# Optimization experiments

Hardware: AMD Instinct MI355X
Metric: run time of the kernel (lower is better)

## Reference

```python
import jax, jax.numpy as jnp
import numpy as np

NUM_NODES = 100000
NUM_EDGES = 600000
NUM_GRAPHS = 512
D = 128  # num_features == latent widths


def setup_inputs() -> dict:
    key = jax.random.key(0)
    ks = jax.random.split(key, 16)
    inp = {
        "x": jax.random.normal(ks[0], (NUM_NODES, D), dtype=jnp.float32),
        "edge_index": jax.random.randint(ks[1], (2, NUM_EDGES), 0, NUM_NODES, dtype=jnp.int32),
        "batch": jnp.sort(jax.random.randint(ks[2], (NUM_NODES,), 0, NUM_GRAPHS, dtype=jnp.int32)),
    }
    s = 1.0 / np.sqrt(D)
    # SAGEConv params per layer: lin_l (applied to mean-aggregated neighbors), lin_r (root), bias
    for i in range(3):
        inp[f"Wl{i+1}"] = jax.random.uniform(ks[3 + 3 * i], (D, D), jnp.float32, -s, s)
        inp[f"Wr{i+1}"] = jax.random.uniform(ks[4 + 3 * i], (D, D), jnp.float32, -s, s)
        inp[f"b{i+1}"] = jax.random.uniform(ks[5 + 3 * i], (D,), jnp.float32, -s, s)
    inp["Wro"] = jax.random.uniform(ks[12], (D, 1), jnp.float32, -s, s)
    inp["bro"] = jax.random.uniform(ks[13], (1,), jnp.float32, -s, s)
    return inp


def _sage_conv(h, Wl, Wr, b, src, dst):
    # mean aggregation of source features at destination nodes
    msg = jax.ops.segment_sum(h[src], dst, num_segments=NUM_NODES)          # [N, D]
    cnt = jax.ops.segment_sum(jnp.ones((src.shape[0], 1), h.dtype), dst,
                              num_segments=NUM_NODES)                        # [N, 1]
    mean = msg / jnp.maximum(cnt, 1.0)
    return mean @ Wl + h @ Wr + b


def reference(x, edge_index, batch, Wl1, Wr1, b1, Wl2, Wr2, b2, Wl3, Wr3, b3, Wro, bro):
    src, dst = edge_index[0], edge_index[1]
    h = x
    for Wl, Wr, b in ((Wl1, Wr1, b1), (Wl2, Wr2, b2), (Wl3, Wr3, b3)):
        h = jax.nn.relu(_sage_conv(h, Wl, Wr, b, src, dst))
    # per-graph sum pooling (replaces the python loop over unique batch ids)
    pooled = jax.ops.segment_sum(h, batch, num_segments=NUM_GRAPHS)  # [G, D]
    return jax.nn.sigmoid(pooled @ Wro + bro)  # [G, 1]
```

## Files before the change

### kernel.cpp

```cpp
#include <hip/hip_runtime.h>
#include <math.h>

#define N_NODES 100000
#define N_EDGES 600000
#define N_GRAPHS 512
#define D 128
#define SCAN_BS 1024
#define SCAN_NBC ((N_NODES + SCAN_BS - 1) / SCAN_BS)
#define NPART 8
#define PART_SZ (N_NODES / NPART)
#define E4 (N_EDGES / 4)
#define SPLIT_B 12500

typedef unsigned short u16;
typedef __attribute__((ext_vector_type(8))) short short8;
typedef __attribute__((ext_vector_type(4))) float f32x4;

__device__ __forceinline__ u16 f2bf(float f) {
    unsigned int u = __float_as_uint(f);
    u += 0x7FFFu + ((u >> 16) & 1u);
    return (u16)(u >> 16);
}
__device__ __forceinline__ float bf2f(u16 h) {
    return __uint_as_float(((unsigned int)h) << 16);
}
__device__ __forceinline__ void split2(float f, unsigned int& h16, unsigned int& l16) {
    unsigned int u = __float_as_uint(f);
    unsigned int hb = (u + (0x7FFFu + ((u >> 16) & 1u))) & 0xffff0000u;
    float lo = f - __uint_as_float(hb);
    unsigned int ul = __float_as_uint(lo);
    h16 = hb >> 16;
    l16 = (ul + (0x7FFFu + ((ul >> 16) & 1u))) >> 16;
}

typedef __attribute__((address_space(1))) const unsigned int gas_u32;
typedef __attribute__((address_space(3))) unsigned int las_u32;
__device__ __forceinline__ void gload16(const void* g, void* l) {
    __builtin_amdgcn_global_load_lds((gas_u32*)g, (las_u32*)l, 16, 0, 0);
}

__global__ __launch_bounds__(256) void zero_i_kernel(int* __restrict__ p, int n) {
    int i = blockIdx.x * 256 + threadIdx.x;
    if (i < n) p[i] = 0;
}

__global__ __launch_bounds__(256) void hist_kernel(const int* __restrict__ dst,
                                                   int* __restrict__ deg) {
    int e = blockIdx.x * 256 + threadIdx.x;
    if (e < N_EDGES) atomicAdd(&deg[dst[e]], 1);
}

__global__ __launch_bounds__(1024) void scan1_kernel(const int* __restrict__ deg,
                                                     int* __restrict__ excl,
                                                     int* __restrict__ blocksum) {
    __shared__ int buf[2][SCAN_BS];
    const int t = threadIdx.x;
    const int gid = blockIdx.x * SCAN_BS + t;
    int v = (gid < N_NODES) ? deg[gid] : 0;
    buf[0][t] = v;
    __syncthreads();
    int pi = 0;
    for (int off = 1; off < SCAN_BS; off <<= 1) {
        int val = buf[pi][t];
        if (t >= off) val += buf[pi][t - off];
        buf[pi ^ 1][t] = val;
        pi ^= 1;
        __syncthreads();
    }
    int incl = buf[pi][t];
    if (gid < N_NODES) excl[gid] = incl - v;
    if (t == SCAN_BS - 1) blocksum[blockIdx.x] = incl;
}

__global__ __launch_bounds__(256) void scan3_kernel(const int* __restrict__ excl,
                                                    const int* __restrict__ blocksum,
                                                    int* __restrict__ rowptr) {
    __shared__ int buf[2][128];
    const int t = threadIdx.x;
    if (t < 128) buf[0][t] = (t < SCAN_NBC) ? blocksum[t] : 0;
    __syncthreads();
    int pi = 0;
    for (int off = 1; off < 128; off <<= 1) {
        if (t < 128) {
            int val = buf[pi][t];
            if (t >= off) val += buf[pi][t - off];
            buf[pi ^ 1][t] = val;
        }
        pi ^= 1;
        __syncthreads();
    }
    const int i = blockIdx.x * 256 + t;
    if (i < N_NODES) {
        const int j = i / SCAN_BS;
        const int pref = (j == 0) ? 0 : buf[pi][j - 1];
        rowptr[i] = excl[i] + pref;
    }
    if (i == 0) rowptr[N_NODES] = N_EDGES;
}

__global__ __launch_bounds__(256) void fill_kernel(const int* __restrict__ src,
                                                   const int* __restrict__ dst,
                                                   const int* __restrict__ rowptr,
                                                   int* __restrict__ fill,
                                                   int* __restrict__ csr_src) {
    const int lo = (blockIdx.x & (NPART - 1)) * PART_SZ;
    const int i4 = (blockIdx.x >> 3) * 256 + threadIdx.x;
    if (i4 >= E4) return;
    const int4 d4 = ((const int4*)dst)[i4];
    const int4 s4 = ((const int4*)src)[i4];
    if ((unsigned)(d4.x - lo) < (unsigned)PART_SZ) {
        int pos = rowptr[d4.x] + atomicAdd(&fill[d4.x], 1);
        csr_src[pos] = s4.x;
    }
    if ((unsigned)(d4.y - lo) < (unsigned)PART_SZ) {
        int pos = rowptr[d4.y] + atomicAdd(&fill[d4.y], 1);
        csr_src[pos] = s4.y;
    }
    if ((unsigned)(d4.z - lo) < (unsigned)PART_SZ) {
        int pos = rowptr[d4.z] + atomicAdd(&fill[d4.z], 1);
        csr_src[pos] = s4.z;
    }
    if ((unsigned)(d4.w - lo) < (unsigned)PART_SZ) {
        int pos = rowptr[d4.w] + atomicAdd(&fill[d4.w], 1);
        csr_src[pos] = s4.w;
    }
}

__global__ __launch_bounds__(256) void prep_kernel(const float* __restrict__ x,
                                                   u16* __restrict__ Hhi,
                                                   u16* __restrict__ Hlo,
                                                   const float* __restrict__ Wl1, const float* __restrict__ Wr1,
                                                   const float* __restrict__ Wl2, const float* __restrict__ Wr2,
                                                   const float* __restrict__ Wl3, const float* __restrict__ Wr3,
                                                   u16* __restrict__ wph, u16* __restrict__ wpl) {
    if (blockIdx.x < SPLIT_B) {
        const int i = blockIdx.x * 256 + threadIdx.x;
        const float4 v = ((const float4*)x)[i];
        unsigned int h0, l0, h1, l1, h2, l2, h3, l3;
        split2(v.x, h0, l0); split2(v.y, h1, l1);
        split2(v.z, h2, l2); split2(v.w, h3, l3);
        uint2 oh, ol;
        oh.x = h0 | (h1 << 16); oh.y = h2 | (h3 << 16);
        ol.x = l0 | (l1 << 16); ol.y = l2 | (l3 << 16);
        ((uint2*)Hhi)[i] = oh;
        ((uint2*)Hlo)[i] = ol;
    } else {
        const int b = (blockIdx.x - SPLIT_B) * 4 + (threadIdx.x >> 6);
        const int lane = threadIdx.x & 63;
        const int layer = b >> 6;
        const int t = b & 63;
        const float* Wl = (layer == 0) ? Wl1 : (layer == 1) ? Wl2 : Wl3;
        const float* Wr = (layer == 0) ? Wr1 : (layer == 1) ? Wr2 : Wr3;
        const int nt = t >> 3, kt = t & 7;
        const int n = nt * 16 + (lane & 15);
        const int k0 = kt * 32 + (lane >> 4) * 8;
        const size_t base = (size_t)layer * 32768 + (size_t)(t * 64 + lane) * 8;
        #pragma unroll
        for (int j = 0; j < 8; ++j) {
            const int k = k0 + j;
            const float w = (k < 128) ? Wl[k * 128 + n] : Wr[(k - 128) * 128 + n];
            const u16 h = f2bf(w);
            wph[base + j] = h;
            wpl[base + j] = f2bf(w - bf2f(h));
        }
    }
}

__global__ __launch_bounds__(512, 4) void gemm_kernel(const u16* __restrict__ INhi,
                                                      const u16* __restrict__ INlo,
                                                      const int* __restrict__ rowptr,
                                                      const int* __restrict__ csr_src,
                                                      const u16* __restrict__ Wph,
                                                      const u16* __restrict__ Wpl,
                                                      const float* __restrict__ bias,
                                                      u16* __restrict__ OHhi,
                                                      u16* __restrict__ OHlo,
                                                      const float* __restrict__ Wro,
                                                      float* rowdot) {
    __shared__ uint4 ldsAll[5120];
    const int t = threadIdx.x;
    const int lane = t & 63;
    const int wv = t >> 6;
    const int m0 = blockIdx.x * 128 + wv * 16;
    const int row16 = m0 + (lane & 15);
    int rm = row16; if (rm >= N_NODES) rm = 0;
    const int ko = (lane >> 4) * 8;

    int beg = 0, deg = 0;
    if (row16 < N_NODES) {
        beg = rowptr[row16];
        deg = rowptr[row16 + 1] - beg;
    }

#define STAGE_W(Q, B) do {                                                      \
        const uint4* gh_ = (const uint4*)Wph + (Q) * 1024;                      \
        const uint4* gl_ = (const uint4*)Wpl + (Q) * 1024;                      \
        _Pragma("unroll")                                                       \
        for (int i_ = 0; i_ < 2; ++i_) {                                        \
            gload16(gh_ + t + 512 * i_,                                         \
                    (void*)&ldsAll[(B) * 2048 + wv * 64 + 512 * i_]);           \
            gload16(gl_ + t + 512 * i_,                                         \
                    (void*)&ldsAll[(B) * 2048 + 1024 + wv * 64 + 512 * i_]);    \
        }                                                                       \
    } while (0)

    STAGE_W(0, 0);
    __builtin_amdgcn_sched_barrier(0);
    STAGE_W(1, 1);
    __builtin_amdgcn_sched_barrier(0);

    short8 ah[4], al[4];
    #pragma unroll
    for (int kt = 0; kt < 4; ++kt) {
        ah[kt] = *(const short8*)(INhi + (size_t)rm * D + kt * 32 + ko);
        al[kt] = *(const short8*)(INlo + (size_t)rm * D + kt * 32 + ko);
    }

    float ac[4][8];
    #pragma unroll
    for (int kt = 0; kt < 4; ++kt) {
        #pragma unroll
        for (int j = 0; j < 8; ++j) ac[kt][j] = 0.f;
    }
    int s_cur = (deg > 0) ? csr_src[beg] : 0;
    for (int n = 0; __any(n < deg); ++n) {
        const bool act = n < deg;
        const int s_nxt = (n + 1 < deg) ? csr_src[beg + n + 1] : 0;
        if (act) {
            const size_t rb = (size_t)s_cur * D + ko;
            #pragma unroll
            for (int kt = 0; kt < 4; ++kt) {
                const uint4 v = *(const uint4*)(INhi + rb + kt * 32);
                ac[kt][0] += __uint_as_float(v.x << 16);
                ac[kt][1] += __uint_as_float(v.x & 0xffff0000u);
                ac[kt][2] += __uint_as_float(v.y << 16);
                ac[kt][3] += __uint_as_float(v.y & 0xffff0000u);
                ac[kt][4] += __uint_as_float(v.z << 16);
                ac[kt][5] += __uint_as_float(v.z & 0xffff0000u);
                ac[kt][6] += __uint_as_float(v.w << 16);
                ac[kt][7] += __uint_as_float(v.w & 0xffff0000u);
            }
        }
        s_cur = s_nxt;
    }
    const float inv = 1.0f / (float)max(deg, 1);
    short8 am[4];
    #pragma unroll
    for (int kt = 0; kt < 4; ++kt) {
        uint4 u;
        u.x = (unsigned)f2bf(ac[kt][0] * inv) | ((unsigned)f2bf(ac[kt][1] * inv) << 16);
        u.y = (unsigned)f2bf(ac[kt][2] * inv) | ((unsigned)f2bf(ac[kt][3] * inv) << 16);
        u.z = (unsigned)f2bf(ac[kt][4] * inv) | ((unsigned)f2bf(ac[kt][5] * inv) << 16);
        u.w = (unsigned)f2bf(ac[kt][6] * inv) | ((unsigned)f2bf(ac[kt][7] * inv) << 16);
        am[kt] = __builtin_bit_cast(short8, u);
    }
    __builtin_amdgcn_sched_barrier(0);

    const int cl = lane & 15;
    const int g4 = (lane >> 4) << 2;
    char* bounceB = (char*)ldsAll + 65536 + wv * 2048;

    f32x4 acc8[2][4];

#define COMPUTE_S(Q, B) do {                                                    \
        const u16* bufU_ = (const u16*)(ldsAll + (B) * 2048);                   \
        _Pragma("unroll")                                                       \
        for (int l_ = 0; l_ < 2; ++l_) {                                        \
            f32x4 acc_ = {0.f, 0.f, 0.f, 0.f};                                  \
            _Pragma("unroll")                                                   \
            for (int kt_ = 0; kt_ < 8; ++kt_) {                                 \
                const int fo_ = (l_ * 8 + kt_) * 512 + lane * 8;                \
                const short8 bh_ = *(const short8*)(bufU_ + fo_);               \
                const short8 bl_ = *(const short8*)(bufU_ + 8192 + fo_);        \
                if (kt_ < 4) {                                                  \
                    acc_ = __builtin_amdgcn_mfma_f32_16x16x32_bf16(am[kt_], bh_, acc_, 0, 0, 0); \
                    acc_ = __builtin_amdgcn_mfma_f32_16x16x32_bf16(am[kt_], bl_, acc_, 0, 0, 0); \
                } else {                                                        \
                    acc_ = __builtin_amdgcn_mfma_f32_16x16x32_bf16(ah[kt_ - 4], bh_, acc_, 0, 0, 0); \
                    acc_ = __builtin_amdgcn_mfma_f32_16x16x32_bf16(ah[kt_ - 4], bl_, acc_, 0, 0, 0); \
                    acc_ = __builtin_amdgcn_mfma_f32_16x16x32_bf16(al[kt_ - 4], bh_, acc_, 0, 0, 0); \
                }                                                               \
            }                                                                   \
            acc8[(Q) >> 1][((Q) & 1) * 2 + l_] = acc_;                          \
        }                                                                       \
    } while (0)

    asm volatile("s_waitcnt vmcnt(0)" ::: "memory");
    __builtin_amdgcn_s_barrier();
    COMPUTE_S(0, 0);
    __builtin_amdgcn_s_barrier();
    STAGE_W(2, 0);
    COMPUTE_S(1, 1);
    __builtin_amdgcn_s_barrier();
    STAGE_W(3, 1);
    asm volatile("s_waitcnt vmcnt(4)" ::: "memory");
    __builtin_amdgcn_s_barrier();
    COMPUTE_S(2, 0);
    asm volatile("s_waitcnt vmcnt(0)" ::: "memory");
    __builtin_amdgcn_s_barrier();
    COMPUTE_S(3, 1);

    if (rowdot) {
        float wsum[4] = {0.f, 0.f, 0.f, 0.f};
        #pragma unroll
        for (int si = 0; si < 2; ++si) {
            #pragma unroll
            for (int nt2 = 0; nt2 < 4; ++nt2) {
                const int col = (si * 4 + nt2) * 16 + cl;
                const float bv = bias[col];
                const float wroc = Wro[col];
                #pragma unroll
                for (int r = 0; r < 4; ++r) {
                    const float v = fmaxf(acc8[si][nt2][r] + bv, 0.f);
                    wsum[r] = fmaf(v, wroc, wsum[r]);
                }
            }
        }
        #pragma unroll
        for (int r = 0; r < 4; ++r) {
            float tsum = wsum[r];
            tsum += __shfl_down(tsum, 8, 64);
            tsum += __shfl_down(tsum, 4, 64);
            tsum += __shfl_down(tsum, 2, 64);
            tsum += __shfl_down(tsum, 1, 64);
            const int row = m0 + g4 + r;
            if (cl == 0 && row < N_NODES) {
                rowdot[row] = tsum;
            }
        }
    } else {
        #pragma unroll
        for (int si = 0; si < 2; ++si) {
            asm volatile("s_waitcnt lgkmcnt(0)" ::: "memory");
            unsigned int lo_pack[8];
            #pragma unroll
            for (int nt2 = 0; nt2 < 4; ++nt2) {
                const int col = (si * 4 + nt2) * 16 + cl;
                const float bv = bias[col];
                #pragma unroll
                for (int r = 0; r < 4; ++r) {
                    const int rr = g4 + r;
                    const float v = fmaxf(acc8[si][nt2][r] + bv, 0.f);
                    unsigned int h16, l16;
                    split2(v, h16, l16);
                    const int boff = (rr * 128 + (nt2 * 16 + cl) * 2) ^ ((rr & 7) << 4);
                    *(u16*)(bounceB + boff) = (u16)h16;
                    if (r & 1) lo_pack[nt2 * 2 + (r >> 1)] |= l16 << 16;
                    else       lo_pack[nt2 * 2 + (r >> 1)]  = l16;
                }
            }
            asm volatile("s_waitcnt lgkmcnt(0)" ::: "memory");
            #pragma unroll
            for (int j = 0; j < 2; ++j) {
                const int rr = j * 8 + (lane >> 3);
                const int blk = lane & 7;
                const uint4 vv = *(const uint4*)(bounceB + rr * 128 + ((blk ^ (rr & 7)) << 4));
                const int grow = m0 + rr;
                if (grow < N_NODES)
                    *(uint4*)(OHhi + (size_t)grow * D + si * 64 + blk * 8) = vv;
            }
            asm volatile("s_waitcnt lgkmcnt(0)" ::: "memory");
            #pragma unroll
            for (int nt2 = 0; nt2 < 4; ++nt2) {
                #pragma unroll
                for (int r = 0; r < 4; ++r) {
                    const int rr = g4 + r;
                    const unsigned int l16 = (lo_pack[nt2 * 2 + (r >> 1)] >> ((r & 1) * 16)) & 0xffffu;
                    const int boff = (rr * 128 + (nt2 * 16 + cl) * 2) ^ ((rr & 7) << 4);
                    *(u16*)(bounceB + boff) = (u16)l16;
                }
            }
            asm volatile("s_waitcnt lgkmcnt(0)" ::: "memory");
            #pragma unroll
            for (int j = 0; j < 2; ++j) {
                const int rr = j * 8 + (lane >> 3);
                const int blk = lane & 7;
                const uint4 vv = *(const uint4*)(bounceB + rr * 128 + ((blk ^ (rr & 7)) << 4));
                const int grow = m0 + rr;
                if (grow < N_NODES)
                    *(uint4*)(OHlo + (size_t)grow * D + si * 64 + blk * 8) = vv;
            }
        }
    }
#undef STAGE_W
#undef COMPUTE_S
}

__global__ __launch_bounds__(64) void final_kernel(const float* __restrict__ rowdot,
                                                   const int* __restrict__ batch,
                                                   const float* __restrict__ bro,
                                                   float* __restrict__ out) {
    const int g = blockIdx.x;
    const int t = threadIdx.x;
    int lo = 0, hi = N_NODES;
    while (lo < hi) { int mid = (lo + hi) >> 1; if (batch[mid] < g) lo = mid + 1; else hi = mid; }
    int lo2 = lo, hi2 = N_NODES;
    while (lo2 < hi2) { int mid = (lo2 + hi2) >> 1; if (batch[mid] < g + 1) lo2 = mid + 1; else hi2 = mid; }

    float acc = 0.0f;
    for (int i = lo + t; i < lo2; i += 64) acc += rowdot[i];
    #pragma unroll
    for (int off = 32; off > 0; off >>= 1) acc += __shfl_down(acc, off, 64);
    if (t == 0) out[g] = 1.0f / (1.0f + expf(-(acc + bro[0])));
}

extern "C" void kernel_launch(void* const* d_in, const int* in_sizes, int n_in,
                              void* d_out, int out_size, void* d_ws, size_t ws_size,
                              hipStream_t stream) {
    const float* x     = (const float*)d_in[0];
    const int*   ei    = (const int*)d_in[1];
    const int*   batch = (const int*)d_in[2];
    const int*   src   = ei;
    const int*   dst   = ei + N_EDGES;
    const float* Wl[3] = {(const float*)d_in[3], (const float*)d_in[6], (const float*)d_in[9]};
    const float* Wr[3] = {(const float*)d_in[4], (const float*)d_in[7], (const float*)d_in[10]};
    const float* bs[3] = {(const float*)d_in[5], (const float*)d_in[8], (const float*)d_in[11]};
    const float* Wro   = (const float*)d_in[12];
    const float* bro   = (const float*)d_in[13];
    float* out = (float*)d_out;

    const size_t ND = (size_t)N_NODES * D;
    char* ws = (char*)d_ws;
    u16* Ahi = (u16*)ws;
    u16* Alo = Ahi + ND;
    u16* Bhi = Alo + ND;
    u16* Blo = Bhi + ND;
    u16* Wph = Blo + ND;
    u16* Wpl = Wph + 3 * 32768;
    int* deg      = (int*)(Wpl + 3 * 32768);
    int* fill     = deg + N_NODES;
    float* rowdot = (float*)(fill + N_NODES);
    int* excl     = (int*)(rowdot + N_NODES);
    int* blocksum = excl + N_NODES;
    int* rowptr   = blocksum + 128;
    int* csr_src  = rowptr + N_NODES + 1;

    const int EB      = (N_EDGES + 255) / 256;
    const int NB      = (N_NODES + 255) / 256;
    const int NB2     = (2 * N_NODES + 255) / 256;
    const int EPB     = ((E4 + 255) / 256) * NPART;
    const int PREP_B  = SPLIT_B + 48;
    const int GEMM_B  = (N_NODES + 127) / 128;

    zero_i_kernel<<<NB2, 256, 0, stream>>>(deg, 2 * N_NODES);
    hist_kernel<<<EB, 256, 0, stream>>>(dst, deg);
    scan1_kernel<<<SCAN_NBC, SCAN_BS, 0, stream>>>(deg, excl, blocksum);
    scan3_kernel<<<NB, 256, 0, stream>>>(excl, blocksum, rowptr);
    fill_kernel<<<EPB, 256, 0, stream>>>(src, dst, rowptr, fill, csr_src);

    prep_kernel<<<PREP_B, 256, 0, stream>>>(x, Ahi, Alo,
                                            Wl[0], Wr[0], Wl[1], Wr[1], Wl[2], Wr[2],
                                            Wph, Wpl);

    gemm_kernel<<<GEMM_B, 512, 0, stream>>>(Ahi, Alo, rowptr, csr_src,
                                            Wph, Wpl, bs[0],
                                            Bhi, Blo, Wro, (float*)nullptr);
    gemm_kernel<<<GEMM_B, 512, 0, stream>>>(Bhi, Blo, rowptr, csr_src,
                                            Wph + 32768, Wpl + 32768, bs[1],
                                            Ahi, Alo, Wro, (float*)nullptr);
    gemm_kernel<<<GEMM_B, 512, 0, stream>>>(Ahi, Alo, rowptr, csr_src,
                                            Wph + 2 * 32768, Wpl + 2 * 32768, bs[2],
                                            Bhi, Blo, Wro, rowdot);

    final_kernel<<<N_GRAPHS, 64, 0, stream>>>(rowdot, batch, bro, out);
}
```

Baseline: 363.6 us.

## Halve weight staging chunks to shrink LDS footprint and deepen pipeline

Weight staging into LDS now uses 8 chunks of 16 output columns each instead of 4 chunks of 32, so the shared buffer shrinks from 80 KB to 32 KB. The bounce buffer is moved to alias the weight buffers after compute finishes. The aim is to raise occupancy per CU, since the launch bounds ask for 4 blocks of 512 threads. In exchange there are more barriers and waitcnt stages, with less compute between each load and its use.

```diff
diff --git a/kernel.cpp b/kernel.cpp
--- a/kernel.cpp
+++ b/kernel.cpp
@@ -177,7 +177,7 @@
                                                       u16* __restrict__ OHlo,
                                                       const float* __restrict__ Wro,
                                                       float* rowdot) {
-    __shared__ uint4 ldsAll[5120];
+    __shared__ uint4 ldsAll[2048];
     const int t = threadIdx.x;
     const int lane = t & 63;
     const int wv = t >> 6;
@@ -193,15 +193,10 @@
     }
 
 #define STAGE_W(Q, B) do {                                                      \
-        const uint4* gh_ = (const uint4*)Wph + (Q) * 1024;                      \
-        const uint4* gl_ = (const uint4*)Wpl + (Q) * 1024;                      \
-        _Pragma("unroll")                                                       \
-        for (int i_ = 0; i_ < 2; ++i_) {                                        \
-            gload16(gh_ + t + 512 * i_,                                         \
-                    (void*)&ldsAll[(B) * 2048 + wv * 64 + 512 * i_]);           \
-            gload16(gl_ + t + 512 * i_,                                         \
-                    (void*)&ldsAll[(B) * 2048 + 1024 + wv * 64 + 512 * i_]);    \
-        }                                                                       \
+        const uint4* gh_ = (const uint4*)Wph + (Q) * 512;                       \
+        const uint4* gl_ = (const uint4*)Wpl + (Q) * 512;                       \
+        gload16(gh_ + t, (void*)&ldsAll[(B) * 1024 + wv * 64]);                 \
+        gload16(gl_ + t, (void*)&ldsAll[(B) * 1024 + 512 + wv * 64]);           \
     } while (0)
 
     STAGE_W(0, 0);
@@ -258,31 +253,27 @@
 
     const int cl = lane & 15;
     const int g4 = (lane >> 4) << 2;
-    char* bounceB = (char*)ldsAll + 65536 + wv * 2048;
 
     f32x4 acc8[2][4];
 
 #define COMPUTE_S(Q, B) do {                                                    \
-        const u16* bufU_ = (const u16*)(ldsAll + (B) * 2048);                   \
+        const u16* bufU_ = (const u16*)(ldsAll + (B) * 1024);                   \
+        f32x4 acc_ = {0.f, 0.f, 0.f, 0.f};                                      \
         _Pragma("unroll")                                                       \
-        for (int l_ = 0; l_ < 2; ++l_) {                                        \
-            f32x4 acc_ = {0.f, 0.f, 0.f, 0.f};                                  \
-            _Pragma("unroll")                                                   \
-            for (int kt_ = 0; kt_ < 8; ++kt_) {                                 \
-                const int fo_ = (l_ * 8 + kt_) * 512 + lane * 8;                \
-                const short8 bh_ = *(const short8*)(bufU_ + fo_);               \
-                const short8 bl_ = *(const short8*)(bufU_ + 8192 + fo_);        \
-                if (kt_ < 4) {                                                  \
-                    acc_ = __builtin_amdgcn_mfma_f32_16x16x32_bf16(am[kt_], bh_, acc_, 0, 0, 0); \
-                    acc_ = __builtin_amdgcn_mfma_f32_16x16x32_bf16(am[kt_], bl_, acc_, 0, 0, 0); \
-                } else {                                                        \
-                    acc_ = __builtin_amdgcn_mfma_f32_16x16x32_bf16(ah[kt_ - 4], bh_, acc_, 0, 0, 0); \
-                    acc_ = __builtin_amdgcn_mfma_f32_16x16x32_bf16(ah[kt_ - 4], bl_, acc_, 0, 0, 0); \
-                    acc_ = __builtin_amdgcn_mfma_f32_16x16x32_bf16(al[kt_ - 4], bh_, acc_, 0, 0, 0); \
-                }                                                               \
+        for (int kt_ = 0; kt_ < 8; ++kt_) {                                     \
+            const int fo_ = kt_ * 512 + lane * 8;                               \
+            const short8 bh_ = *(const short8*)(bufU_ + fo_);                   \
+            const short8 bl_ = *(const short8*)(bufU_ + 4096 + fo_);            \
+            if (kt_ < 4) {                                                      \
+                acc_ = __builtin_amdgcn_mfma_f32_16x16x32_bf16(am[kt_], bh_, acc_, 0, 0, 0); \
+                acc_ = __builtin_amdgcn_mfma_f32_16x16x32_bf16(am[kt_], bl_, acc_, 0, 0, 0); \
+            } else {                                                            \
+                acc_ = __builtin_amdgcn_mfma_f32_16x16x32_bf16(ah[kt_ - 4], bh_, acc_, 0, 0, 0); \
+                acc_ = __builtin_amdgcn_mfma_f32_16x16x32_bf16(ah[kt_ - 4], bl_, acc_, 0, 0, 0); \
+                acc_ = __builtin_amdgcn_mfma_f32_16x16x32_bf16(al[kt_ - 4], bh_, acc_, 0, 0, 0); \
             }                                                                   \
-            acc8[(Q) >> 1][((Q) & 1) * 2 + l_] = acc_;                          \
         }                                                                       \
+        acc8[(Q) >> 2][(Q) & 3] = acc_;                                         \
     } while (0)
 
     asm volatile("s_waitcnt vmcnt(0)" ::: "memory");
@@ -290,15 +281,38 @@
     COMPUTE_S(0, 0);
     __builtin_amdgcn_s_barrier();
     STAGE_W(2, 0);
+    __builtin_amdgcn_sched_barrier(0);
     COMPUTE_S(1, 1);
     __builtin_amdgcn_s_barrier();
     STAGE_W(3, 1);
-    asm volatile("s_waitcnt vmcnt(4)" ::: "memory");
+    asm volatile("s_waitcnt vmcnt(2)" ::: "memory");
     __builtin_amdgcn_s_barrier();
     COMPUTE_S(2, 0);
+    __builtin_amdgcn_s_barrier();
+    STAGE_W(4, 0);
+    asm volatile("s_waitcnt vmcnt(2)" ::: "memory");
+    __builtin_amdgcn_s_barrier();
+    COMPUTE_S(3, 1);
+    __builtin_amdgcn_s_barrier();
+    STAGE_W(5, 1);
+    asm volatile("s_waitcnt vmcnt(2)" ::: "memory");
+    __builtin_amdgcn_s_barrier();
+    COMPUTE_S(4, 0);
+    __builtin_amdgcn_s_barrier();
+    STAGE_W(6, 0);
+    asm volatile("s_waitcnt vmcnt(2)" ::: "memory");
+    __builtin_amdgcn_s_barrier();
+    COMPUTE_S(5, 1);
+    __builtin_amdgcn_s_barrier();
+    STAGE_W(7, 1);
+    asm volatile("s_waitcnt vmcnt(2)" ::: "memory");
+    __builtin_amdgcn_s_barrier();
+    COMPUTE_S(6, 0);
     asm volatile("s_waitcnt vmcnt(0)" ::: "memory");
     __builtin_amdgcn_s_barrier();
-    COMPUTE_S(3, 1);
+    COMPUTE_S(7, 1);
+
+    char* bounceB = (char*)ldsAll + wv * 2048;
 
     if (rowdot) {
         float wsum[4] = {0.f, 0.f, 0.f, 0.f};
```

New measurement: 362.2 us. About the same (-0.4%).
